# Performance work log

Measured on AMD Instinct MI355X. Metric: run time of the kernel, lower is better.

Reference implementation:

```python
import jax, jax.numpy as jnp
import numpy as np

B, S, E, H, NCTX = 32, 4095, 1024, 16, 4096  # cache len S, new seq_len = S+1
HD = E // H

def setup_inputs() -> dict:
    key = jax.random.key(0)
    ks = jax.random.split(key, 8)
    return {
        "hidden_states": jax.random.normal(ks[0], (B, 1, E), jnp.float32),
        "key_cache": jax.random.normal(ks[1], (B, S, E), jnp.float32),
        "value_cache": jax.random.normal(ks[2], (B, S, E), jnp.float32),
        "attention_mask": jnp.ones((B, S + 1), jnp.int32),
        "c_attn_w": jax.random.normal(ks[3], (E, 3 * E), jnp.float32) * 0.02,
        "c_attn_b": jax.random.normal(ks[4], (3 * E,), jnp.float32) * 0.02,
        "c_proj_w": jax.random.normal(ks[5], (E, E), jnp.float32) * 0.02,
        "c_proj_b": jax.random.normal(ks[6], (E,), jnp.float32) * 0.02,
        "attn_bias": jax.random.normal(ks[7], (NCTX, NCTX), jnp.float32) * 0.02,
    }

def reference(hidden_states, key_cache, value_cache, attention_mask,
              c_attn_w, c_attn_b, c_proj_w, c_proj_b, attn_bias):
    b, _, e = hidden_states.shape
    h, hd = H, E // H
    seq_len = key_cache.shape[1] + 1
    # fused qkv projection on the single decode token
    qkv = hidden_states[:, 0, :] @ c_attn_w + c_attn_b          # [B, 3E]
    q, k, v = jnp.split(qkv, 3, axis=-1)                         # each [B, E]
    # last valid position in attention_mask (index of last 1)
    rev = attention_mask[:, ::-1]
    last = attention_mask.shape[1] - jnp.argmax(rev, axis=1) - 1  # [B]
    # append zero column then scatter new k/v at per-batch last position
    zcol = jnp.zeros((b, 1, e), key_cache.dtype)
    bidx = jnp.arange(b)
    new_k = jnp.concatenate([key_cache, zcol], axis=1).at[bidx, last].set(k)   # [B, seq_len, E]
    new_v = jnp.concatenate([value_cache, zcol], axis=1).at[bidx, last].set(v)
    # multi-head attention with q_len = 1
    qh = q.reshape(b, h, hd)                                     # [B, H, hd]
    kh = new_k.reshape(b, seq_len, h, hd)                        # [B, S+1, H, hd]
    vh = new_v.reshape(b, seq_len, h, hd)
    scores = jnp.einsum('bhd,bshd->bhs', qh, kh) / jnp.sqrt(jnp.float32(hd))  # [B, H, S+1]
    scores = scores + attn_bias[0, :seq_len][None, None, :]
    scores = jnp.where(attention_mask[:, None, :] == 0, jnp.float32(-1e9), scores)
    w = jax.nn.softmax(scores, axis=-1)
    ctx = jnp.einsum('bhs,bshd->bhd', w, vh).reshape(b, 1, e)    # [B, 1, E]
    out = ctx @ c_proj_w + c_proj_b                               # resid_dropout is eval no-op
    return out, new_k, new_v
```

## Files before the change

kernel.cpp:

```cpp
#include <hip/hip_runtime.h>
#include <hip/hip_bf16.h>

typedef float f32x4 __attribute__((ext_vector_type(4)));

#define BATCH 32
#define S_LEN 4095
#define SEQ   4096
#define E_DIM 1024
#define NH    16
#define HD    64

__device__ __forceinline__ f32x4 ntload4(const float* p) {
    return __builtin_nontemporal_load((const f32x4*)p);
}
__device__ __forceinline__ void ntstore4(float* p, f32x4 v) {
    __builtin_nontemporal_store(v, (f32x4*)p);
}

__global__ __launch_bounds__(256) void prep_kernel(const int* __restrict__ mask,
                                                   const float* __restrict__ bias,
                                                   int* __restrict__ lastbuf,
                                                   float* __restrict__ mbias) {
    int b = blockIdx.x;
    int t = threadIdx.x;
    int best = -1;
    for (int s = t; s < SEQ; s += 256) {
        int mv = mask[b * SEQ + s];
        mbias[b * SEQ + s] = mv ? bias[s] : -1.0e9f;
        if (mv) best = max(best, s);
    }
    __shared__ int red[256];
    red[t] = best;
    __syncthreads();
    for (int o = 128; o > 0; o >>= 1) {
        if (t < o) red[t] = max(red[t], red[t + o]);
        __syncthreads();
    }
    if (t == 0) lastbuf[b] = (red[0] < 0) ? (SEQ - 1) : red[0];
}

__global__ __launch_bounds__(256) void qkv_kernel(const float* __restrict__ hs,
                                                  const float* __restrict__ W,
                                                  const float* __restrict__ bias,
                                                  float* __restrict__ qkv) {
    const int b = blockIdx.y;
    const int jj = threadIdx.x & 63;
    const int j = blockIdx.x * 64 + jj;
    const int ksl = threadIdx.x >> 6;
    __shared__ float h[E_DIM];
    for (int i = threadIdx.x; i < E_DIM; i += 256) h[i] = hs[b * E_DIM + i];
    __syncthreads();
    float acc = 0.f;
    const int k0 = ksl * 256;
    #pragma unroll 8
    for (int k = k0; k < k0 + 256; ++k) acc = fmaf(h[k], W[(size_t)k * 3072 + j], acc);
    __shared__ float red[4][64];
    red[ksl][jj] = acc;
    __syncthreads();
    if (ksl == 0)
        qkv[b * 3072 + j] = acc + red[1][jj] + red[2][jj] + red[3][jj] + bias[j];
}

template <int CHUNK_T>
__global__ __launch_bounds__(256) void attn_k_kernel(
    const float* __restrict__ kcache, const float* __restrict__ mbias,
    const float* __restrict__ qkv, const int* __restrict__ lastbuf,
    float* __restrict__ newk, float* __restrict__ wts) {
    const int b = blockIdx.y;
    const int chunk = blockIdx.x;
    const int t = threadIdx.x;
    const int wave = t >> 6;
    const int lane = t & 63;
    const int head = wave * 4 + (lane >> 4);
    const int lig = lane & 15;
    const int col = head * HD + lig * 4;
    const int last = lastbuf[b];

    const f32x4 q4 = *(const f32x4*)(qkv + b * 3072 + col);
    const f32x4 kn4 = *(const f32x4*)(qkv + b * 3072 + 1024 + col);
    const float* kb = kcache + (size_t)b * S_LEN * E_DIM;
    float* nkb = newk + (size_t)b * SEQ * E_DIM;
    const float* mbb = mbias + b * SEQ;

    __shared__ float sc[NH][CHUNK_T];
    const int s0 = chunk * CHUNK_T;
    const bool clean = (s0 + CHUNK_T <= S_LEN) && (last < s0 || last >= s0 + CHUNK_T);

    if (clean) {
        for (int r = 0; r < CHUNK_T; r += 8) {
            f32x4 kk[8];
            #pragma unroll
            for (int u = 0; u < 8; ++u)
                kk[u] = ntload4(kb + (size_t)(s0 + r + u) * E_DIM + col);
            #pragma unroll
            for (int u = 0; u < 8; ++u)
                ntstore4(nkb + (size_t)(s0 + r + u) * E_DIM + col, kk[u]);
            #pragma unroll
            for (int u = 0; u < 8; ++u) {
                float p = kk[u][0] * q4[0] + kk[u][1] * q4[1] + kk[u][2] * q4[2] + kk[u][3] * q4[3];
                p += __shfl_xor(p, 1);
                p += __shfl_xor(p, 2);
                p += __shfl_xor(p, 4);
                p += __shfl_xor(p, 8);
                if (lig == 0) sc[head][r + u] = __expf(fmaf(p, 0.125f, mbb[s0 + r + u]));
            }
        }
    } else {
        for (int r = 0; r < CHUNK_T; ++r) {
            const int s = s0 + r;
            f32x4 kk;
            if (s == last) kk = kn4;
            else if (s < S_LEN) kk = ntload4(kb + (size_t)s * E_DIM + col);
            else kk = (f32x4){0.f, 0.f, 0.f, 0.f};
            ntstore4(nkb + (size_t)s * E_DIM + col, kk);
            float p = kk[0] * q4[0] + kk[1] * q4[1] + kk[2] * q4[2] + kk[3] * q4[3];
            p += __shfl_xor(p, 1);
            p += __shfl_xor(p, 2);
            p += __shfl_xor(p, 4);
            p += __shfl_xor(p, 8);
            if (lig == 0) sc[head][r] = __expf(fmaf(p, 0.125f, mbb[s]));
        }
    }
    __syncthreads();
    for (int i = t; i < NH * CHUNK_T; i += 256) {
        const int h2 = i / CHUNK_T, r = i % CHUNK_T;
        wts[(size_t)(b * NH + h2) * SEQ + s0 + r] = sc[h2][r];
    }
}

template <int CHUNK_T>
__global__ __launch_bounds__(256) void attn_v_kernel(
    const float* __restrict__ vcache, const float* __restrict__ wts,
    const float* __restrict__ qkv, const int* __restrict__ lastbuf,
    float* __restrict__ newv, float* __restrict__ pl, float* __restrict__ pctx) {
    constexpr int NCHUNK_T = SEQ / CHUNK_T;
    const int b = blockIdx.y;
    const int chunk = blockIdx.x;
    const int t = threadIdx.x;
    const int wave = t >> 6;
    const int lane = t & 63;
    const int head = wave * 4 + (lane >> 4);
    const int lig = lane & 15;
    const int col = head * HD + lig * 4;
    const int last = lastbuf[b];

    const f32x4 vn4 = *(const f32x4*)(qkv + b * 3072 + 2048 + col);
    const float* vb = vcache + (size_t)b * S_LEN * E_DIM;
    float* nvb = newv + (size_t)b * SEQ * E_DIM;

    __shared__ float w_s[NH][CHUNK_T];
    const int s0 = chunk * CHUNK_T;
    for (int i = t; i < NH * CHUNK_T; i += 256) {
        const int h2 = i / CHUNK_T, r = i % CHUNK_T;
        w_s[h2][r] = wts[(size_t)(b * NH + h2) * SEQ + s0 + r];
    }
    __syncthreads();

    float l = 0.f;
    f32x4 acc = (f32x4){0.f, 0.f, 0.f, 0.f};
    const bool clean = (s0 + CHUNK_T <= S_LEN) && (last < s0 || last >= s0 + CHUNK_T);

    if (clean) {
        for (int r = 0; r < CHUNK_T; r += 8) {
            f32x4 vv[8];
            #pragma unroll
            for (int u = 0; u < 8; ++u)
                vv[u] = ntload4(vb + (size_t)(s0 + r + u) * E_DIM + col);
            #pragma unroll
            for (int u = 0; u < 8; ++u)
                ntstore4(nvb + (size_t)(s0 + r + u) * E_DIM + col, vv[u]);
            #pragma unroll
            for (int u = 0; u < 8; ++u) {
                const float w = w_s[head][r + u];
                l += w;
                acc += vv[u] * w;
            }
        }
    } else {
        for (int r = 0; r < CHUNK_T; ++r) {
            const int s = s0 + r;
            f32x4 vv;
            if (s == last) vv = vn4;
            else if (s < S_LEN) vv = ntload4(vb + (size_t)s * E_DIM + col);
            else vv = (f32x4){0.f, 0.f, 0.f, 0.f};
            ntstore4(nvb + (size_t)s * E_DIM + col, vv);
            const float w = w_s[head][r];
            l += w;
            acc += vv * w;
        }
    }

    const int pidx = (b * NH + head) * NCHUNK_T + chunk;
    if (lig == 0) pl[pidx] = l;
    *(f32x4*)(pctx + (size_t)pidx * HD + lig * 4) = acc;
}

template <int CHUNK_T>
__global__ __launch_bounds__(256) void attn_fused_kernel(
    const float* __restrict__ kcache, const float* __restrict__ vcache,
    const float* __restrict__ mbias,
    const float* __restrict__ qkv, const int* __restrict__ lastbuf,
    float* __restrict__ newk, float* __restrict__ newv,
    float* __restrict__ pl, float* __restrict__ pctx) {
    constexpr int NCHUNK_T = SEQ / CHUNK_T;
    const int b = blockIdx.y;
    const int chunk = blockIdx.x;
    const int t = threadIdx.x;
    const int wave = t >> 6;
    const int lane = t & 63;
    const int head = wave * 4 + (lane >> 4);
    const int lig = lane & 15;
    const int col = head * HD + lig * 4;
    const int last = lastbuf[b];

    const f32x4 q4 = *(const f32x4*)(qkv + b * 3072 + col);
    const f32x4 kn4 = *(const f32x4*)(qkv + b * 3072 + 1024 + col);
    const f32x4 vn4 = *(const f32x4*)(qkv + b * 3072 + 2048 + col);
    const float* kb = kcache + (size_t)b * S_LEN * E_DIM;
    const float* vb = vcache + (size_t)b * S_LEN * E_DIM;
    float* nkb = newk + (size_t)b * SEQ * E_DIM;
    float* nvb = newv + (size_t)b * SEQ * E_DIM;
    const float* mbb = mbias + b * SEQ;

    float l = 0.f;
    f32x4 acc = (f32x4){0.f, 0.f, 0.f, 0.f};
    const int s0 = chunk * CHUNK_T;
    for (int r = 0; r < CHUNK_T; ++r) {
        const int s = s0 + r;
        f32x4 kk, vv;
        if (s == last) { kk = kn4; vv = vn4; }
        else if (s < S_LEN) {
            kk = ntload4(kb + (size_t)s * E_DIM + col);
            vv = ntload4(vb + (size_t)s * E_DIM + col);
        } else { kk = (f32x4){0.f, 0.f, 0.f, 0.f}; vv = kk; }
        ntstore4(nkb + (size_t)s * E_DIM + col, kk);
        ntstore4(nvb + (size_t)s * E_DIM + col, vv);
        float p = kk[0] * q4[0] + kk[1] * q4[1] + kk[2] * q4[2] + kk[3] * q4[3];
        p += __shfl_xor(p, 1);
        p += __shfl_xor(p, 2);
        p += __shfl_xor(p, 4);
        p += __shfl_xor(p, 8);
        const float w = __expf(fmaf(p, 0.125f, mbb[s]));
        l += w;
        acc += vv * w;
    }
    const int pidx = (b * NH + head) * NCHUNK_T + chunk;
    if (lig == 0) pl[pidx] = l;
    *(f32x4*)(pctx + (size_t)pidx * HD + lig * 4) = acc;
}

__global__ __launch_bounds__(256) void reduce_kernel(const float* __restrict__ pl,
                                                     const float* __restrict__ pctx,
                                                     float* __restrict__ ctxout,
                                                     int nchunk) {
    const int gw = (blockIdx.x * blockDim.x + threadIdx.x) >> 6;
    const int lane = threadIdx.x & 63;
    if (gw >= BATCH * NH) return;
    float lacc = 0.f, cacc = 0.f;
    for (int c = 0; c < nchunk; ++c) {
        lacc += pl[gw * nchunk + c];
        cacc += pctx[(size_t)(gw * nchunk + c) * HD + lane];
    }
    ctxout[gw * HD + lane] = cacc / lacc;
}

__global__ __launch_bounds__(256) void proj_kernel(const float* __restrict__ ctx,
                                                   const float* __restrict__ W,
                                                   const float* __restrict__ bias,
                                                   float* __restrict__ out) {
    const int b = blockIdx.y;
    const int jj = threadIdx.x & 63;
    const int j = blockIdx.x * 64 + jj;
    const int ksl = threadIdx.x >> 6;
    __shared__ float h[E_DIM];
    for (int i = threadIdx.x; i < E_DIM; i += 256) h[i] = ctx[b * E_DIM + i];
    __syncthreads();
    float acc = 0.f;
    const int k0 = ksl * 256;
    #pragma unroll 8
    for (int k = k0; k < k0 + 256; ++k) acc = fmaf(h[k], W[(size_t)k * E_DIM + j], acc);
    __shared__ float red[4][64];
    red[ksl][jj] = acc;
    __syncthreads();
    if (ksl == 0)
        out[b * E_DIM + j] = acc + red[1][jj] + red[2][jj] + red[3][jj] + bias[j];
}

extern "C" void kernel_launch(void* const* d_in, const int* in_sizes, int n_in,
                              void* d_out, int out_size, void* d_ws, size_t ws_size,
                              hipStream_t stream) {
    const float* hs      = (const float*)d_in[0];
    const float* kcache  = (const float*)d_in[1];
    const float* vcache  = (const float*)d_in[2];
    const int*   mask    = (const int*)d_in[3];
    const float* attn_w  = (const float*)d_in[4];
    const float* attn_b  = (const float*)d_in[5];
    const float* proj_w  = (const float*)d_in[6];
    const float* proj_b  = (const float*)d_in[7];
    const float* bias0   = (const float*)d_in[8];

    float* out0 = (float*)d_out;
    float* newk = out0 + (size_t)BATCH * E_DIM;
    float* newv = newk + (size_t)BATCH * SEQ * E_DIM;

    float* ws = (float*)d_ws;
    float* qkv    = ws;
    float* ctxbuf = qkv + 98304;
    float* mbias  = ctxbuf + 32768;

    const size_t base = 98304 + 32768 + 131072;
    const size_t need_split = (base + 2097152ull + 32768 + 2097152ull + 32) * 4;
    const bool use_split = ws_size >= need_split;

    if (use_split) {
        float* wts     = mbias + 131072;
        float* pl      = wts + 2097152;
        float* pctx    = pl + 32768;
        int*   lastbuf = (int*)(pctx + 2097152);

        prep_kernel<<<dim3(BATCH), dim3(256), 0, stream>>>(mask, bias0, lastbuf, mbias);
        qkv_kernel<<<dim3(48, BATCH), dim3(256), 0, stream>>>(hs, attn_w, attn_b, qkv);
        attn_k_kernel<64><<<dim3(64, BATCH), dim3(256), 0, stream>>>(
            kcache, mbias, qkv, lastbuf, newk, wts);
        attn_v_kernel<64><<<dim3(64, BATCH), dim3(256), 0, stream>>>(
            vcache, wts, qkv, lastbuf, newv, pl, pctx);
        reduce_kernel<<<dim3((BATCH * NH * 64 + 255) / 256), dim3(256), 0, stream>>>(
            pl, pctx, ctxbuf, 64);
        proj_kernel<<<dim3(16, BATCH), dim3(256), 0, stream>>>(ctxbuf, proj_w, proj_b, out0);
    } else {
        float* pl      = mbias + 131072;
        float* pctx    = pl + 16384;
        int*   lastbuf = (int*)(pctx + 1048576);

        prep_kernel<<<dim3(BATCH), dim3(256), 0, stream>>>(mask, bias0, lastbuf, mbias);
        qkv_kernel<<<dim3(48, BATCH), dim3(256), 0, stream>>>(hs, attn_w, attn_b, qkv);
        attn_fused_kernel<128><<<dim3(32, BATCH), dim3(256), 0, stream>>>(
            kcache, vcache, mbias, qkv, lastbuf, newk, newv, pl, pctx);
        reduce_kernel<<<dim3((BATCH * NH * 64 + 255) / 256), dim3(256), 0, stream>>>(
            pl, pctx, ctxbuf, 32);
        proj_kernel<<<dim3(16, BATCH), dim3(256), 0, stream>>>(ctxbuf, proj_w, proj_b, out0);
    }
}
```

Before: 471.1 us.

## Interleave K/V row assignment across blocks and use regular loads instead of nontemporal

Each attention block now handles 8 groups of 8 consecutive rows strided by 512, replacing one contiguous 64-row chunk, so concurrently running blocks touch neighbouring memory regions. Cache loads switch from nontemporal to ordinary loads, and the unroll drops from 8 to 4 rows per group. The weights buffer is now laid out per block, so the V pass reads one contiguous slab. This targets DRAM page and channel locality for the bandwidth-bound cache copy, at the risk of losing the cache-bypass behaviour of nontemporal loads.

```diff
diff --git a/kernel.cpp b/kernel.cpp
--- a/kernel.cpp
+++ b/kernel.cpp
@@ -10,9 +10,6 @@
 #define NH    16
 #define HD    64
 
-__device__ __forceinline__ f32x4 ntload4(const float* p) {
-    return __builtin_nontemporal_load((const f32x4*)p);
-}
 __device__ __forceinline__ void ntstore4(float* p, f32x4 v) {
     __builtin_nontemporal_store(v, (f32x4*)p);
 }
@@ -61,11 +58,157 @@
         qkv[b * 3072 + j] = acc + red[1][jj] + red[2][jj] + red[3][jj] + bias[j];
 }
 
-template <int CHUNK_T>
 __global__ __launch_bounds__(256) void attn_k_kernel(
     const float* __restrict__ kcache, const float* __restrict__ mbias,
     const float* __restrict__ qkv, const int* __restrict__ lastbuf,
     float* __restrict__ newk, float* __restrict__ wts) {
+    const int c = blockIdx.x;
+    const int b = blockIdx.y;
+    const int t = threadIdx.x;
+    const int wave = t >> 6;
+    const int lane = t & 63;
+    const int head = wave * 4 + (lane >> 4);
+    const int lig = lane & 15;
+    const int col = head * HD + lig * 4;
+    const int last = lastbuf[b];
+
+    const f32x4 q4 = *(const f32x4*)(qkv + b * 3072 + col);
+    const f32x4 kn4 = *(const f32x4*)(qkv + b * 3072 + 1024 + col);
+    const float* kb = kcache + (size_t)b * S_LEN * E_DIM;
+    float* nkb = newk + (size_t)b * SEQ * E_DIM;
+    const float* mbb = mbias + b * SEQ;
+
+    __shared__ float sc[NH][64];
+    const bool clean = (((last >> 3) & 63) != c) && (c != 63);
+
+    if (clean) {
+        for (int i = 0; i < 8; ++i) {
+            const int sb = 8 * c + 512 * i;
+            #pragma unroll
+            for (int g = 0; g < 8; g += 4) {
+                f32x4 kk[4];
+                #pragma unroll
+                for (int u = 0; u < 4; ++u)
+                    kk[u] = *(const f32x4*)(kb + (size_t)(sb + g + u) * E_DIM + col);
+                #pragma unroll
+                for (int u = 0; u < 4; ++u)
+                    ntstore4(nkb + (size_t)(sb + g + u) * E_DIM + col, kk[u]);
+                #pragma unroll
+                for (int u = 0; u < 4; ++u) {
+                    float p = kk[u][0] * q4[0] + kk[u][1] * q4[1] + kk[u][2] * q4[2] + kk[u][3] * q4[3];
+                    p += __shfl_xor(p, 1);
+                    p += __shfl_xor(p, 2);
+                    p += __shfl_xor(p, 4);
+                    p += __shfl_xor(p, 8);
+                    if (lig == 0)
+                        sc[head][i * 8 + g + u] = __expf(fmaf(p, 0.125f, mbb[sb + g + u]));
+                }
+            }
+        }
+    } else {
+        for (int i = 0; i < 8; ++i) {
+            #pragma unroll
+            for (int u = 0; u < 8; ++u) {
+                const int s = 8 * c + 512 * i + u;
+                f32x4 kk;
+                if (s == last) kk = kn4;
+                else if (s < S_LEN) kk = *(const f32x4*)(kb + (size_t)s * E_DIM + col);
+                else kk = (f32x4){0.f, 0.f, 0.f, 0.f};
+                ntstore4(nkb + (size_t)s * E_DIM + col, kk);
+                float p = kk[0] * q4[0] + kk[1] * q4[1] + kk[2] * q4[2] + kk[3] * q4[3];
+                p += __shfl_xor(p, 1);
+                p += __shfl_xor(p, 2);
+                p += __shfl_xor(p, 4);
+                p += __shfl_xor(p, 8);
+                if (lig == 0)
+                    sc[head][i * 8 + u] = __expf(fmaf(p, 0.125f, mbb[s]));
+            }
+        }
+    }
+    __syncthreads();
+    float* wblk = wts + (size_t)(b * 64 + c) * (NH * 64);
+    for (int idx = t; idx < NH * 64; idx += 256)
+        wblk[idx] = sc[idx >> 6][idx & 63];
+}
+
+__global__ __launch_bounds__(256) void attn_v_kernel(
+    const float* __restrict__ vcache, const float* __restrict__ wts,
+    const float* __restrict__ qkv, const int* __restrict__ lastbuf,
+    float* __restrict__ newv, float* __restrict__ pl, float* __restrict__ pctx) {
+    const int c = blockIdx.x;
+    const int b = blockIdx.y;
+    const int t = threadIdx.x;
+    const int wave = t >> 6;
+    const int lane = t & 63;
+    const int head = wave * 4 + (lane >> 4);
+    const int lig = lane & 15;
+    const int col = head * HD + lig * 4;
+    const int last = lastbuf[b];
+
+    const f32x4 vn4 = *(const f32x4*)(qkv + b * 3072 + 2048 + col);
+    const float* vb = vcache + (size_t)b * S_LEN * E_DIM;
+    float* nvb = newv + (size_t)b * SEQ * E_DIM;
+
+    __shared__ float w_s[NH][64];
+    const float* wblk = wts + (size_t)(b * 64 + c) * (NH * 64);
+    for (int idx = t; idx < NH * 64; idx += 256)
+        w_s[idx >> 6][idx & 63] = wblk[idx];
+    __syncthreads();
+
+    float l = 0.f;
+    f32x4 acc = (f32x4){0.f, 0.f, 0.f, 0.f};
+    const bool clean = (((last >> 3) & 63) != c) && (c != 63);
+
+    if (clean) {
+        for (int i = 0; i < 8; ++i) {
+            const int sb = 8 * c + 512 * i;
+            #pragma unroll
+            for (int g = 0; g < 8; g += 4) {
+                f32x4 vv[4];
+                #pragma unroll
+                for (int u = 0; u < 4; ++u)
+                    vv[u] = *(const f32x4*)(vb + (size_t)(sb + g + u) * E_DIM + col);
+                #pragma unroll
+                for (int u = 0; u < 4; ++u)
+                    ntstore4(nvb + (size_t)(sb + g + u) * E_DIM + col, vv[u]);
+                #pragma unroll
+                for (int u = 0; u < 4; ++u) {
+                    const float w = w_s[head][i * 8 + g + u];
+                    l += w;
+                    acc += vv[u] * w;
+                }
+            }
+        }
+    } else {
+        for (int i = 0; i < 8; ++i) {
+            #pragma unroll
+            for (int u = 0; u < 8; ++u) {
+                const int s = 8 * c + 512 * i + u;
+                f32x4 vv;
+                if (s == last) vv = vn4;
+                else if (s < S_LEN) vv = *(const f32x4*)(vb + (size_t)s * E_DIM + col);
+                else vv = (f32x4){0.f, 0.f, 0.f, 0.f};
+                ntstore4(nvb + (size_t)s * E_DIM + col, vv);
+                const float w = w_s[head][i * 8 + u];
+                l += w;
+                acc += vv * w;
+            }
+        }
+    }
+
+    const int pidx = (b * NH + head) * 64 + c;
+    if (lig == 0) pl[pidx] = l;
+    *(f32x4*)(pctx + (size_t)pidx * HD + lig * 4) = acc;
+}
+
+template <int CHUNK_T>
+__global__ __launch_bounds__(256) void attn_fused_kernel(
+    const float* __restrict__ kcache, const float* __restrict__ vcache,
+    const float* __restrict__ mbias,
+    const float* __restrict__ qkv, const int* __restrict__ lastbuf,
+    float* __restrict__ newk, float* __restrict__ newv,
+    float* __restrict__ pl, float* __restrict__ pctx) {
+    constexpr int NCHUNK_T = SEQ / CHUNK_T;
     const int b = blockIdx.y;
     const int chunk = blockIdx.x;
     const int t = threadIdx.x;
@@ -78,143 +221,6 @@
 
     const f32x4 q4 = *(const f32x4*)(qkv + b * 3072 + col);
     const f32x4 kn4 = *(const f32x4*)(qkv + b * 3072 + 1024 + col);
-    const float* kb = kcache + (size_t)b * S_LEN * E_DIM;
-    float* nkb = newk + (size_t)b * SEQ * E_DIM;
-    const float* mbb = mbias + b * SEQ;
-
-    __shared__ float sc[NH][CHUNK_T];
-    const int s0 = chunk * CHUNK_T;
-    const bool clean = (s0 + CHUNK_T <= S_LEN) && (last < s0 || last >= s0 + CHUNK_T);
-
-    if (clean) {
-        for (int r = 0; r < CHUNK_T; r += 8) {
-            f32x4 kk[8];
-            #pragma unroll
-            for (int u = 0; u < 8; ++u)
-                kk[u] = ntload4(kb + (size_t)(s0 + r + u) * E_DIM + col);
-            #pragma unroll
-            for (int u = 0; u < 8; ++u)
-                ntstore4(nkb + (size_t)(s0 + r + u) * E_DIM + col, kk[u]);
-            #pragma unroll
-            for (int u = 0; u < 8; ++u) {
-                float p = kk[u][0] * q4[0] + kk[u][1] * q4[1] + kk[u][2] * q4[2] + kk[u][3] * q4[3];
-                p += __shfl_xor(p, 1);
-                p += __shfl_xor(p, 2);
-                p += __shfl_xor(p, 4);
-                p += __shfl_xor(p, 8);
-                if (lig == 0) sc[head][r + u] = __expf(fmaf(p, 0.125f, mbb[s0 + r + u]));
-            }
-        }
-    } else {
-        for (int r = 0; r < CHUNK_T; ++r) {
-            const int s = s0 + r;
-            f32x4 kk;
-            if (s == last) kk = kn4;
-            else if (s < S_LEN) kk = ntload4(kb + (size_t)s * E_DIM + col);
-            else kk = (f32x4){0.f, 0.f, 0.f, 0.f};
-            ntstore4(nkb + (size_t)s * E_DIM + col, kk);
-            float p = kk[0] * q4[0] + kk[1] * q4[1] + kk[2] * q4[2] + kk[3] * q4[3];
-            p += __shfl_xor(p, 1);
-            p += __shfl_xor(p, 2);
-            p += __shfl_xor(p, 4);
-            p += __shfl_xor(p, 8);
-            if (lig == 0) sc[head][r] = __expf(fmaf(p, 0.125f, mbb[s]));
-        }
-    }
-    __syncthreads();
-    for (int i = t; i < NH * CHUNK_T; i += 256) {
-        const int h2 = i / CHUNK_T, r = i % CHUNK_T;
-        wts[(size_t)(b * NH + h2) * SEQ + s0 + r] = sc[h2][r];
-    }
-}
-
-template <int CHUNK_T>
-__global__ __launch_bounds__(256) void attn_v_kernel(
-    const float* __restrict__ vcache, const float* __restrict__ wts,
-    const float* __restrict__ qkv, const int* __restrict__ lastbuf,
-    float* __restrict__ newv, float* __restrict__ pl, float* __restrict__ pctx) {
-    constexpr int NCHUNK_T = SEQ / CHUNK_T;
-    const int b = blockIdx.y;
-    const int chunk = blockIdx.x;
-    const int t = threadIdx.x;
-    const int wave = t >> 6;
-    const int lane = t & 63;
-    const int head = wave * 4 + (lane >> 4);
-    const int lig = lane & 15;
-    const int col = head * HD + lig * 4;
-    const int last = lastbuf[b];
-
-    const f32x4 vn4 = *(const f32x4*)(qkv + b * 3072 + 2048 + col);
-    const float* vb = vcache + (size_t)b * S_LEN * E_DIM;
-    float* nvb = newv + (size_t)b * SEQ * E_DIM;
-
-    __shared__ float w_s[NH][CHUNK_T];
-    const int s0 = chunk * CHUNK_T;
-    for (int i = t; i < NH * CHUNK_T; i += 256) {
-        const int h2 = i / CHUNK_T, r = i % CHUNK_T;
-        w_s[h2][r] = wts[(size_t)(b * NH + h2) * SEQ + s0 + r];
-    }
-    __syncthreads();
-
-    float l = 0.f;
-    f32x4 acc = (f32x4){0.f, 0.f, 0.f, 0.f};
-    const bool clean = (s0 + CHUNK_T <= S_LEN) && (last < s0 || last >= s0 + CHUNK_T);
-
-    if (clean) {
-        for (int r = 0; r < CHUNK_T; r += 8) {
-            f32x4 vv[8];
-            #pragma unroll
-            for (int u = 0; u < 8; ++u)
-                vv[u] = ntload4(vb + (size_t)(s0 + r + u) * E_DIM + col);
-            #pragma unroll
-            for (int u = 0; u < 8; ++u)
-                ntstore4(nvb + (size_t)(s0 + r + u) * E_DIM + col, vv[u]);
-            #pragma unroll
-            for (int u = 0; u < 8; ++u) {
-                const float w = w_s[head][r + u];
-                l += w;
-                acc += vv[u] * w;
-            }
-        }
-    } else {
-        for (int r = 0; r < CHUNK_T; ++r) {
-            const int s = s0 + r;
-            f32x4 vv;
-            if (s == last) vv = vn4;
-            else if (s < S_LEN) vv = ntload4(vb + (size_t)s * E_DIM + col);
-            else vv = (f32x4){0.f, 0.f, 0.f, 0.f};
-            ntstore4(nvb + (size_t)s * E_DIM + col, vv);
-            const float w = w_s[head][r];
-            l += w;
-            acc += vv * w;
-        }
-    }
-
-    const int pidx = (b * NH + head) * NCHUNK_T + chunk;
-    if (lig == 0) pl[pidx] = l;
-    *(f32x4*)(pctx + (size_t)pidx * HD + lig * 4) = acc;
-}
-
-template <int CHUNK_T>
-__global__ __launch_bounds__(256) void attn_fused_kernel(
-    const float* __restrict__ kcache, const float* __restrict__ vcache,
-    const float* __restrict__ mbias,
-    const float* __restrict__ qkv, const int* __restrict__ lastbuf,
-    float* __restrict__ newk, float* __restrict__ newv,
-    float* __restrict__ pl, float* __restrict__ pctx) {
-    constexpr int NCHUNK_T = SEQ / CHUNK_T;
-    const int b = blockIdx.y;
-    const int chunk = blockIdx.x;
-    const int t = threadIdx.x;
-    const int wave = t >> 6;
-    const int lane = t & 63;
-    const int head = wave * 4 + (lane >> 4);
-    const int lig = lane & 15;
-    const int col = head * HD + lig * 4;
-    const int last = lastbuf[b];
-
-    const f32x4 q4 = *(const f32x4*)(qkv + b * 3072 + col);
-    const f32x4 kn4 = *(const f32x4*)(qkv + b * 3072 + 1024 + col);
     const f32x4 vn4 = *(const f32x4*)(qkv + b * 3072 + 2048 + col);
     const float* kb = kcache + (size_t)b * S_LEN * E_DIM;
     const float* vb = vcache + (size_t)b * S_LEN * E_DIM;
@@ -230,8 +236,8 @@
         f32x4 kk, vv;
         if (s == last) { kk = kn4; vv = vn4; }
         else if (s < S_LEN) {
-            kk = ntload4(kb + (size_t)s * E_DIM + col);
-            vv = ntload4(vb + (size_t)s * E_DIM + col);
+            kk = *(const f32x4*)(kb + (size_t)s * E_DIM + col);
+            vv = *(const f32x4*)(vb + (size_t)s * E_DIM + col);
         } else { kk = (f32x4){0.f, 0.f, 0.f, 0.f}; vv = kk; }
         ntstore4(nkb + (size_t)s * E_DIM + col, kk);
         ntstore4(nvb + (size_t)s * E_DIM + col, vv);
@@ -320,9 +326,9 @@
 
         prep_kernel<<<dim3(BATCH), dim3(256), 0, stream>>>(mask, bias0, lastbuf, mbias);
         qkv_kernel<<<dim3(48, BATCH), dim3(256), 0, stream>>>(hs, attn_w, attn_b, qkv);
-        attn_k_kernel<64><<<dim3(64, BATCH), dim3(256), 0, stream>>>(
+        attn_k_kernel<<<dim3(64, BATCH), dim3(256), 0, stream>>>(
             kcache, mbias, qkv, lastbuf, newk, wts);
-        attn_v_kernel<64><<<dim3(64, BATCH), dim3(256), 0, stream>>>(
+        attn_v_kernel<<<dim3(64, BATCH), dim3(256), 0, stream>>>(
             vcache, wts, qkv, lastbuf, newv, pl, pctx);
         reduce_kernel<<<dim3((BATCH * NH * 64 + 255) / 256), dim3(256), 0, stream>>>(
             pl, pctx, ctxbuf, 64);
```

After: 571.2 us. 1.21x slower.
